# Kernel optimization log

Measured on AMD Instinct MI355X. Metric: run time of the kernel, lower is better.

Reference implementation:

```python
import jax, jax.numpy as jnp
import numpy as np

ALPHA = 2.6
OPTIMAL_RANK = 1.0
SIGMA = 1.8


def setup_inputs() -> dict:
    key = jax.random.key(0)
    k1, k2 = jax.random.split(key)
    B, D, NP = 2048, 768, 8
    q_reps = jax.random.normal(k1, (B, D), dtype=jnp.float32)
    p_reps = jax.random.normal(k2, (B * NP, D), dtype=jnp.float32)
    return {"q_reps": q_reps, "p_reps": p_reps, "n_passages": NP}


def reference(q_reps, p_reps, n_passages):
    B = q_reps.shape[0]
    # [B, P] contrastive score matrix
    scores = jnp.matmul(q_reps, p_reps.T)
    target = jnp.arange(B, dtype=jnp.int32) * n_passages

    # rank position of the positive passage per query (descending argsort)
    rankings = jnp.argsort(-scores, axis=1)            # [B, P]
    positive_rankings = jnp.argmax(
        rankings == target[:, None], axis=1
    ).astype(jnp.float32)                              # [B]

    # per-sample cross-entropy (reduction='none')
    logp = jax.nn.log_softmax(scores, axis=1)
    raw_loss = -jnp.take_along_axis(logp, target[:, None], axis=1)[:, 0]

    # Gaussian rank weighting: w = 1 + alpha * exp(-(r - r_opt)^2 / (2 sigma^2))
    extra_weight = jnp.exp(-((positive_rankings - OPTIMAL_RANK) ** 2) / (2.0 * SIGMA ** 2))
    weights = 1.0 + ALPHA * extra_weight

    loss = jnp.mean(raw_loss * weights)
    return loss
```

## Files before the change

kernel.cpp:

```cpp
#include <hip/hip_runtime.h>
#include <math.h>


#define BQ 2048
#define DD 768
#define NPASS 8
#define PP 16384
#define BM 256
#define BN 256
#define BK 128
#define KITERS 6
#define NBLK 64
#define MBLK 8
#define NCHUNKS 256

#define ALPHA_C 2.6f
#define INV_2SIG2 (1.0f/6.48f)

typedef __attribute__((ext_vector_type(4))) float floatx4;

#define NQ8   196608
#define NTOT8 1769472
#define NCB   6912
__global__ __launch_bounds__(256) void prep_kernel(const float* __restrict__ qf,
                                                   const float* __restrict__ pf,
                                                   uint2* __restrict__ qb,
                                                   uint2* __restrict__ pb,
                                                   float* __restrict__ st,
                                                   float* __restrict__ out) {
  const int b = blockIdx.x;
  if (b == 0 && threadIdx.x == 0) *out = 0.f;
  if (b < NCB) {
    const int i = b * 256 + threadIdx.x;
    const float4* src; uint2* dst;
    if (i < NQ8) { src = (const float4*)qf + 2 * (size_t)i; dst = qb + i; }
    else { const size_t j = (size_t)i - NQ8; src = (const float4*)pf + 2 * j; dst = pb + j; }
    const float4 a = src[0], c = src[1];
    unsigned lo = __builtin_amdgcn_cvt_pk_fp8_f32(a.x, a.y, 0, 0);
    lo = __builtin_amdgcn_cvt_pk_fp8_f32(a.z, a.w, lo, 1);
    unsigned hi = __builtin_amdgcn_cvt_pk_fp8_f32(c.x, c.y, 0, 0);
    hi = __builtin_amdgcn_cvt_pk_fp8_f32(c.z, c.w, hi, 1);
    uint2 w; w.x = lo; w.y = hi;
    *dst = w;
  } else {
    const int wv = threadIdx.x >> 6, lane = threadIdx.x & 63;
    const int qi = (b - NCB) * 4 + wv;
    const float4* q4 = (const float4*)(qf + (size_t)qi * DD);
    const float4* p4 = (const float4*)(pf + (size_t)qi * NPASS * DD);
    float acc = 0.f;
#pragma unroll
    for (int u = 0; u < 3; ++u) {
      float4 a = q4[lane + 64 * u];
      float4 c = p4[lane + 64 * u];
      acc = fmaf(a.x, c.x, acc);
      acc = fmaf(a.y, c.y, acc);
      acc = fmaf(a.z, c.z, acc);
      acc = fmaf(a.w, c.w, acc);
    }
#pragma unroll
    for (int off = 32; off >= 1; off >>= 1) acc += __shfl_xor(acc, off);
    if (lane == 0) st[qi] = acc;
  }
}

__global__ __launch_bounds__(1024) void gemm_kernel(const unsigned char* __restrict__ qb,
                                                    const unsigned char* __restrict__ pb,
                                                    const float* __restrict__ st,
                                                    float* __restrict__ pm,
                                                    float* __restrict__ pl,
                                                    float* __restrict__ pc) {
  __shared__ unsigned char As[2][32 * 1024];
  __shared__ unsigned char Bs[2][32 * 1024];
  __shared__ float st_lds[BM];

  const int t = threadIdx.x;
  const int lane = t & 63;
  const int wv = t >> 6;
  const int wm = wv >> 2, wn = wv & 3;
  const int bid = blockIdx.x;
  const int xcd = bid & 7;
  const int nb = xcd * 8 + ((bid >> 3) & 7);
  const int mb = bid >> 6;
  const int qbase = mb * BM;
  const int n0 = nb * BN;
  const int lm = lane & 15;
  const int lq = lane >> 4;
  const int lds_lane = lane * 16;

  if (t < BM) st_lds[t] = st[qbase + t];

  floatx4 acc[4][4];
#pragma unroll
  for (int i = 0; i < 4; ++i)
#pragma unroll
    for (int j = 0; j < 4; ++j) acc[i][j] = (floatx4){0.f, 0.f, 0.f, 0.f};

  const size_t arow = (size_t)(qbase + wv * 16 + lm) * DD;
  const size_t brow = (size_t)(n0 + wv * 16 + lm) * DD;

#define STAGE(KT, BUF)                                                          \
  {                                                                             \
    const size_t koff = (size_t)(KT) * BK + lq * 16;                            \
    _Pragma("unroll")                                                           \
    for (int kh = 0; kh < 2; ++kh) {                                            \
      __builtin_amdgcn_global_load_lds(                                         \
          (const __attribute__((address_space(1))) void*)(qb + arow + koff + kh * 64), \
          (__attribute__((address_space(3))) void*)(&As[BUF][(wv * 2 + kh) * 1024] + lds_lane), \
          16, 0, 0);                                                            \
      __builtin_amdgcn_global_load_lds(                                         \
          (const __attribute__((address_space(1))) void*)(pb + brow + koff + kh * 64), \
          (__attribute__((address_space(3))) void*)(&Bs[BUF][(wv * 2 + kh) * 1024] + lds_lane), \
          16, 0, 0);                                                            \
    }                                                                           \
  }

  STAGE(0, 0)
  for (int kt = 0; kt < KITERS; ++kt) {
    const int cb = kt & 1;
    __syncthreads();
    if (kt < KITERS - 1) STAGE(kt + 1, cb ^ 1)
#pragma unroll
    for (int ks = 0; ks < 4; ++ks) {
      const int kh = ks >> 1;
      const int intra = ((ks & 1) * 2 + (lq >> 1)) * 256 + lm * 16 + (lq & 1) * 8;
      long a[4], b[4];
#pragma unroll
      for (int i = 0; i < 4; ++i)
        a[i] = *(const long*)(&As[cb][((wm * 4 + i) * 2 + kh) * 1024] + intra);
#pragma unroll
      for (int j = 0; j < 4; ++j)
        b[j] = *(const long*)(&Bs[cb][((wn * 4 + j) * 2 + kh) * 1024] + intra);
#pragma unroll
      for (int i = 0; i < 4; ++i)
#pragma unroll
        for (int j = 0; j < 4; ++j)
          acc[i][j] = __builtin_amdgcn_mfma_f32_16x16x32_fp8_fp8(a[i], b[j], acc[i][j], 0, 0, 0);
    }
  }

#pragma unroll
  for (int i = 0; i < 4; ++i) {
#pragma unroll
    for (int r = 0; r < 4; ++r) {
      const int rl = wm * 64 + i * 16 + lq * 4 + r;
      float mx = fmaxf(fmaxf(acc[i][0][r], acc[i][1][r]),
                       fmaxf(acc[i][2][r], acc[i][3][r]));
#pragma unroll
      for (int off = 1; off <= 8; off <<= 1) mx = fmaxf(mx, __shfl_xor(mx, off));
      const float stv = st_lds[rl];
      const int qg = qbase + rl;
      const int tcol = qg * NPASS;
      float sum = 0.f, c = 0.f;
#pragma unroll
      for (int j = 0; j < 4; ++j) {
        const float s = acc[i][j][r];
        sum += __expf(s - mx);
        const int cg = n0 + wn * 64 + j * 16 + lm;
        if (s > stv && cg != tcol) c += 1.f;
      }
#pragma unroll
      for (int off = 1; off <= 8; off <<= 1) {
        sum += __shfl_xor(sum, off);
        c += __shfl_xor(c, off);
      }
      if (lm == 0) {
        const int chunk = nb * 4 + wn;
        const size_t idx = (size_t)qg * NCHUNKS + chunk;
        pm[idx] = mx; pl[idx] = sum; pc[idx] = c;
      }
    }
  }
}

__global__ __launch_bounds__(256) void finalize_kernel(const float* __restrict__ st,
                                                       const float* __restrict__ pm,
                                                       const float* __restrict__ pl,
                                                       const float* __restrict__ pc,
                                                       float* __restrict__ out) {
  const int wv = threadIdx.x >> 6, lane = threadIdx.x & 63;
  const int qi = blockIdx.x * 4 + wv;
  float4 m4 = ((const float4*)(pm + (size_t)qi * NCHUNKS))[lane];
  float mx = fmaxf(fmaxf(m4.x, m4.y), fmaxf(m4.z, m4.w));
#pragma unroll
  for (int off = 32; off >= 1; off >>= 1) mx = fmaxf(mx, __shfl_xor(mx, off));
  float4 l4 = ((const float4*)(pl + (size_t)qi * NCHUNKS))[lane];
  float4 c4 = ((const float4*)(pc + (size_t)qi * NCHUNKS))[lane];
  float l = l4.x * __expf(m4.x - mx) + l4.y * __expf(m4.y - mx) +
            l4.z * __expf(m4.z - mx) + l4.w * __expf(m4.w - mx);
  float c = c4.x + c4.y + c4.z + c4.w;
#pragma unroll
  for (int off = 32; off >= 1; off >>= 1) {
    l += __shfl_xor(l, off);
    c += __shfl_xor(c, off);
  }
  float loss = 0.f;
  if (lane == 0) {
    const float raw = logf(l) + mx - st[qi];
    const float dr = c - 1.0f;
    const float w = 1.0f + ALPHA_C * __expf(-(dr * dr) * INV_2SIG2);
    loss = raw * w * (1.0f / (float)BQ);
  }
  __shared__ float red[4];
  if (lane == 0) red[wv] = loss;
  __syncthreads();
  if (threadIdx.x == 0) atomicAdd(out, red[0] + red[1] + red[2] + red[3]);
}

extern "C" void kernel_launch(void* const* d_in, const int* in_sizes, int n_in,
                              void* d_out, int out_size, void* d_ws, size_t ws_size,
                              hipStream_t stream) {
  const float* q = (const float*)d_in[0];
  const float* p = (const float*)d_in[1];
  char* ws = (char*)d_ws;
  unsigned char* qb = (unsigned char*)ws;
  unsigned char* pb = (unsigned char*)(ws + 1572864);
  float* st = (float*)(ws + 14155776);
  float* pm = (float*)(ws + 14163968);
  float* pl = (float*)(ws + 16261120);
  float* pc = (float*)(ws + 18358272);
  float* out = (float*)d_out;

  prep_kernel<<<NCB + BQ / 4, 256, 0, stream>>>(q, p, (uint2*)qb, (uint2*)pb, st, out);
  gemm_kernel<<<NBLK * MBLK, 1024, 0, stream>>>(qb, pb, st, pm, pl, pc);
  finalize_kernel<<<BQ / 4, 256, 0, stream>>>(st, pm, pl, pc, out);
}
```

Measured before the change: 163.7 us.

## Split GEMM into producer/consumer waves with narrower 256x128 tiles

The GEMM block shrinks from 256x256 to 256x128 output tiles, which doubles the grid to 1024 blocks and halves the B shared-memory buffer. It also specialises the waves: 8 waves do MFMA compute and the epilogue, while the other 8 only issue the global-to-LDS loads for the next K-step. The goal is to keep loads off the compute waves and to raise occupancy and parallelism. The cost is more total A-tile traffic, because each A tile is now loaded twice as often. Only half the waves do math, and the loop still uses a full __syncthreads per step.

```diff
diff --git a/kernel.cpp b/kernel.cpp
--- a/kernel.cpp
+++ b/kernel.cpp
@@ -7,10 +7,10 @@
 #define NPASS 8
 #define PP 16384
 #define BM 256
-#define BN 256
+#define BN 128
 #define BK 128
 #define KITERS 6
-#define NBLK 64
+#define NBLK 128
 #define MBLK 8
 #define NCHUNKS 256
 
@@ -70,103 +70,110 @@
                                                     float* __restrict__ pl,
                                                     float* __restrict__ pc) {
   __shared__ unsigned char As[2][32 * 1024];
-  __shared__ unsigned char Bs[2][32 * 1024];
+  __shared__ unsigned char Bs[2][16 * 1024];
   __shared__ float st_lds[BM];
 
   const int t = threadIdx.x;
   const int lane = t & 63;
   const int wv = t >> 6;
-  const int wm = wv >> 2, wn = wv & 3;
   const int bid = blockIdx.x;
   const int xcd = bid & 7;
-  const int nb = xcd * 8 + ((bid >> 3) & 7);
-  const int mb = bid >> 6;
+  const int nb = xcd * 16 + ((bid >> 3) & 15);
+  const int mb = bid >> 7;
   const int qbase = mb * BM;
   const int n0 = nb * BN;
   const int lm = lane & 15;
   const int lq = lane >> 4;
   const int lds_lane = lane * 16;
+  const bool producer = (wv >= 8);
+  const int pw = wv - 8;
 
   if (t < BM) st_lds[t] = st[qbase + t];
-
-  floatx4 acc[4][4];
-#pragma unroll
-  for (int i = 0; i < 4; ++i)
-#pragma unroll
-    for (int j = 0; j < 4; ++j) acc[i][j] = (floatx4){0.f, 0.f, 0.f, 0.f};
-
-  const size_t arow = (size_t)(qbase + wv * 16 + lm) * DD;
-  const size_t brow = (size_t)(n0 + wv * 16 + lm) * DD;
 
 #define STAGE(KT, BUF)                                                          \
   {                                                                             \
-    const size_t koff = (size_t)(KT) * BK + lq * 16;                            \
     _Pragma("unroll")                                                           \
-    for (int kh = 0; kh < 2; ++kh) {                                            \
+    for (int s = 0; s < 6; ++s) {                                               \
+      const int u = pw * 6 + s;                                                 \
+      const int isB = (u >= 32);                                                \
+      const int ul = isB ? (u - 32) : u;                                        \
+      const int rowg = ul >> 1, kh = ul & 1;                                    \
+      const size_t g = (size_t)((isB ? n0 : qbase) + rowg * 16 + lm) * DD       \
+                       + (size_t)(KT) * BK + kh * 64 + lq * 16;                 \
+      unsigned char* dst = (isB ? &Bs[BUF][ul * 1024] : &As[BUF][ul * 1024]);   \
       __builtin_amdgcn_global_load_lds(                                         \
-          (const __attribute__((address_space(1))) void*)(qb + arow + koff + kh * 64), \
-          (__attribute__((address_space(3))) void*)(&As[BUF][(wv * 2 + kh) * 1024] + lds_lane), \
-          16, 0, 0);                                                            \
-      __builtin_amdgcn_global_load_lds(                                         \
-          (const __attribute__((address_space(1))) void*)(pb + brow + koff + kh * 64), \
-          (__attribute__((address_space(3))) void*)(&Bs[BUF][(wv * 2 + kh) * 1024] + lds_lane), \
-          16, 0, 0);                                                            \
+          (const __attribute__((address_space(1))) void*)((isB ? pb : qb) + g), \
+          (__attribute__((address_space(3))) void*)(dst + lds_lane), 16, 0, 0); \
     }                                                                           \
   }
 
-  STAGE(0, 0)
+  floatx4 acc[4][4];
+#pragma unroll
+  for (int i = 0; i < 4; ++i)
+#pragma unroll
+    for (int j = 0; j < 4; ++j) acc[i][j] = (floatx4){0.f, 0.f, 0.f, 0.f};
+
+  const int wm = wv >> 1, wn = wv & 1;
+
+  if (producer) STAGE(0, 0)
   for (int kt = 0; kt < KITERS; ++kt) {
     const int cb = kt & 1;
     __syncthreads();
-    if (kt < KITERS - 1) STAGE(kt + 1, cb ^ 1)
-#pragma unroll
-    for (int ks = 0; ks < 4; ++ks) {
-      const int kh = ks >> 1;
-      const int intra = ((ks & 1) * 2 + (lq >> 1)) * 256 + lm * 16 + (lq & 1) * 8;
-      long a[4], b[4];
-#pragma unroll
-      for (int i = 0; i < 4; ++i)
-        a[i] = *(const long*)(&As[cb][((wm * 4 + i) * 2 + kh) * 1024] + intra);
-#pragma unroll
-      for (int j = 0; j < 4; ++j)
-        b[j] = *(const long*)(&Bs[cb][((wn * 4 + j) * 2 + kh) * 1024] + intra);
-#pragma unroll
-      for (int i = 0; i < 4; ++i)
+    if (producer) {
+      if (kt < KITERS - 1) STAGE(kt + 1, cb ^ 1)
+    } else {
+#pragma unroll
+      for (int ks = 0; ks < 4; ++ks) {
+        const int kh = ks >> 1;
+        const int intra = ((ks & 1) * 2 + (lq >> 1)) * 256 + lm * 16 + (lq & 1) * 8;
+        long a[4], b[4];
+#pragma unroll
+        for (int i = 0; i < 4; ++i)
+          a[i] = *(const long*)(&As[cb][((wm * 4 + i) * 2 + kh) * 1024] + intra);
 #pragma unroll
         for (int j = 0; j < 4; ++j)
-          acc[i][j] = __builtin_amdgcn_mfma_f32_16x16x32_fp8_fp8(a[i], b[j], acc[i][j], 0, 0, 0);
+          b[j] = *(const long*)(&Bs[cb][((wn * 4 + j) * 2 + kh) * 1024] + intra);
+#pragma unroll
+        for (int i = 0; i < 4; ++i)
+#pragma unroll
+          for (int j = 0; j < 4; ++j)
+            acc[i][j] = __builtin_amdgcn_mfma_f32_16x16x32_fp8_fp8(a[i], b[j], acc[i][j], 0, 0, 0);
+      }
     }
   }
-
-#pragma unroll
-  for (int i = 0; i < 4; ++i) {
-#pragma unroll
-    for (int r = 0; r < 4; ++r) {
-      const int rl = wm * 64 + i * 16 + lq * 4 + r;
-      float mx = fmaxf(fmaxf(acc[i][0][r], acc[i][1][r]),
-                       fmaxf(acc[i][2][r], acc[i][3][r]));
-#pragma unroll
-      for (int off = 1; off <= 8; off <<= 1) mx = fmaxf(mx, __shfl_xor(mx, off));
-      const float stv = st_lds[rl];
-      const int qg = qbase + rl;
-      const int tcol = qg * NPASS;
-      float sum = 0.f, c = 0.f;
-#pragma unroll
-      for (int j = 0; j < 4; ++j) {
-        const float s = acc[i][j][r];
-        sum += __expf(s - mx);
-        const int cg = n0 + wn * 64 + j * 16 + lm;
-        if (s > stv && cg != tcol) c += 1.f;
-      }
-#pragma unroll
-      for (int off = 1; off <= 8; off <<= 1) {
-        sum += __shfl_xor(sum, off);
-        c += __shfl_xor(c, off);
-      }
-      if (lm == 0) {
-        const int chunk = nb * 4 + wn;
-        const size_t idx = (size_t)qg * NCHUNKS + chunk;
-        pm[idx] = mx; pl[idx] = sum; pc[idx] = c;
+#undef STAGE
+
+  if (!producer) {
+#pragma unroll
+    for (int i = 0; i < 4; ++i) {
+#pragma unroll
+      for (int r = 0; r < 4; ++r) {
+        const int rl = wm * 64 + i * 16 + lq * 4 + r;
+        float mx = fmaxf(fmaxf(acc[i][0][r], acc[i][1][r]),
+                         fmaxf(acc[i][2][r], acc[i][3][r]));
+#pragma unroll
+        for (int off = 1; off <= 8; off <<= 1) mx = fmaxf(mx, __shfl_xor(mx, off));
+        const float stv = st_lds[rl];
+        const int qg = qbase + rl;
+        const int tcol = qg * NPASS;
+        float sum = 0.f, c = 0.f;
+#pragma unroll
+        for (int j = 0; j < 4; ++j) {
+          const float s = acc[i][j][r];
+          sum += __expf(s - mx);
+          const int cg = n0 + wn * 64 + j * 16 + lm;
+          if (s > stv && cg != tcol) c += 1.f;
+        }
+#pragma unroll
+        for (int off = 1; off <= 8; off <<= 1) {
+          sum += __shfl_xor(sum, off);
+          c += __shfl_xor(c, off);
+        }
+        if (lm == 0) {
+          const int chunk = nb * 2 + wn;
+          const size_t idx = (size_t)qg * NCHUNKS + chunk;
+          pm[idx] = mx; pl[idx] = sum; pc[idx] = c;
+        }
       }
     }
   }
```

Result: slower. 176.9 us (+8.1%).
